# Performance work log

Measured on AMD Instinct MI355X. Metric: run time of the kernel, lower is better.

Reference implementation:

```python
import jax, jax.numpy as jnp
import numpy as np

A = 2048          # number of atoms
IN_DEPTH = 64
OUT_DEPTH = 64
FILTER_LEN = 12


def setup_inputs() -> dict:
    key = jax.random.key(0)
    k1, k2, k3, k4, k5 = jax.random.split(key, 5)
    node_property_tensor = jax.random.normal(k1, (A, IN_DEPTH), dtype=jnp.float32)
    # connectivity acts as a dense (soft) gather matrix: (A, A, FILTER_LEN)
    connectivity_tensor = jax.random.uniform(k2, (A, A, FILTER_LEN), dtype=jnp.float32)
    bond_property_tensor = jax.random.normal(k3, (A, FILTER_LEN, 2), dtype=jnp.float32)
    # parameters initialized as in the torch module: normal * 0.01
    property_filters = jax.random.normal(k4, (OUT_DEPTH, FILTER_LEN, IN_DEPTH), dtype=jnp.float32) * 0.01
    bond_filters = jax.random.normal(k5, (OUT_DEPTH, FILTER_LEN, 3), dtype=jnp.float32) * 0.01
    return {
        "node_property_tensor": node_property_tensor,
        "connectivity_tensor": connectivity_tensor,
        "bond_property_tensor": bond_property_tensor,
        "property_filters": property_filters,
        "bond_filters": bond_filters,
    }


def reference(node_property_tensor, connectivity_tensor, bond_property_tensor,
              property_filters, bond_filters):
    # node_connection[a, f, i] = sum_n conn[a, n, f] * x[n, i]
    node_connection = jnp.einsum('anf,ni->afi', connectivity_tensor, node_property_tensor)
    # bond_score[a, o, f] = sum_i node_connection[a, f, i] * property_filters[o, f, i]
    bond_score = jnp.einsum('afi,ofi->aof', node_connection, property_filters)
    # combined[a, o, f, :] = [bond_score, bond_prop0, bond_prop1]; multiply by
    # bond_filters[o, f, :] and sum over (f, channel). Split channel 0 (score)
    # from channels 1:3 (bond properties) to avoid materializing the concat.
    out = jnp.einsum('aof,of->ao', bond_score, bond_filters[:, :, 0])
    out = out + jnp.einsum('afc,ofc->ao', bond_property_tensor, bond_filters[:, :, 1:])
    return out  # (A, OUT_DEPTH)
```

## Files before the change

kernel.cpp:

```cpp
#include <hip/hip_runtime.h>


#define NATOM 2048
#define IN_D 64
#define OUT_D 64
#define FLEN 12
#define KTOT (NATOM * FLEN)
#define KSPLIT 32
#define KCHUNK (KTOT / KSPLIT)
#define BM 64
#define KS 64
#define NITER (KCHUNK / KS)
#define LDSW 72

typedef __attribute__((ext_vector_type(8))) short short8;
typedef __attribute__((ext_vector_type(4))) float f32x4;
typedef __attribute__((ext_vector_type(8))) unsigned short u16x8;
typedef __attribute__((ext_vector_type(4))) unsigned short u16x4;

__device__ __forceinline__ void split_bf16(float x, unsigned short& h, unsigned short& l) {
    unsigned int u = __builtin_bit_cast(unsigned int, x);
    unsigned int r = u + 0x7fffu + ((u >> 16) & 1u);
    h = (unsigned short)(r >> 16);
    float hf = __builtin_bit_cast(float, r & 0xffff0000u);
    float res = x - hf;
    unsigned int u2 = __builtin_bit_cast(unsigned int, res);
    l = (unsigned short)((u2 + 0x7fffu + ((u2 >> 16) & 1u)) >> 16);
}

__global__ __launch_bounds__(256) void compute_w_kernel(
    const float* __restrict__ x,
    const float* __restrict__ pf,
    const float* __restrict__ bf,
    unsigned short* __restrict__ wt_hi,
    unsigned short* __restrict__ wt_lo)
{
    __shared__ float x_lds[64][66];
    const int t = threadIdx.x;
    const int ob = blockIdx.x & 15;
    const int nb = blockIdx.x >> 4;

    {
        const int r = t >> 2;
        const int i0 = (t & 3) * 16;
        const float* src = x + (nb * 64 + r) * IN_D + i0;
        #pragma unroll
        for (int j = 0; j < 4; ++j) {
            float4 v = *(const float4*)(src + 4 * j);
            x_lds[r][i0 + 4 * j + 0] = v.x;
            x_lds[r][i0 + 4 * j + 1] = v.y;
            x_lds[r][i0 + 4 * j + 2] = v.z;
            x_lds[r][i0 + 4 * j + 3] = v.w;
        }
    }
    __syncthreads();

    const int l = t & 63;
    const int o = ob * 4 + (t >> 6);
    const int n = nb * 64 + l;

    float acc[FLEN];
    #pragma unroll
    for (int f = 0; f < FLEN; ++f) acc[f] = 0.f;

    for (int i = 0; i < IN_D; i += 4) {
        float x0 = x_lds[l][i + 0], x1 = x_lds[l][i + 1];
        float x2 = x_lds[l][i + 2], x3 = x_lds[l][i + 3];
        #pragma unroll
        for (int f = 0; f < FLEN; ++f) {
            float4 p = *(const float4*)(pf + (o * FLEN + f) * IN_D + i);
            acc[f] += p.x * x0 + p.y * x1 + p.z * x2 + p.w * x3;
        }
    }

    unsigned short hi[FLEN], lo[FLEN];
    #pragma unroll
    for (int f = 0; f < FLEN; ++f) {
        float wv = acc[f] * bf[(o * FLEN + f) * 3 + 0];
        split_bf16(wv, hi[f], lo[f]);
    }
    unsigned short* dh = wt_hi + o * KTOT + n * FLEN;
    unsigned short* dl = wt_lo + o * KTOT + n * FLEN;
    #pragma unroll
    for (int q = 0; q < 3; ++q) {
        u16x4 vh = { hi[4*q], hi[4*q+1], hi[4*q+2], hi[4*q+3] };
        u16x4 vl = { lo[4*q], lo[4*q+1], lo[4*q+2], lo[4*q+3] };
        *(u16x4*)(dh + 4 * q) = vh;
        *(u16x4*)(dl + 4 * q) = vl;
    }
}

__global__ __launch_bounds__(256, 4) void main_gemm_kernel(
    const float* __restrict__ conn,
    const unsigned short* __restrict__ wt_hi,
    const unsigned short* __restrict__ wt_lo,
    float* __restrict__ partials)
{
    __shared__ unsigned short lds[4][BM][LDSW];

    const int t = threadIdx.x;
    const int mblk = blockIdx.x & 31;
    const int kblk = blockIdx.x >> 5;
    const int mBase = mblk * BM;
    const int kBase = kblk * KCHUNK;

    const int r = t >> 2;
    const int p = t & 3;
    const int l = t & 63;
    const int w = t >> 6;
    const int lr = l & 15;
    const int g = l >> 4;

    f32x4 acc[4];
    #pragma unroll
    for (int nbt = 0; nbt < 4; ++nbt) acc[nbt] = 0.f;

    const float* connRow = conn + (long)(mBase + r) * KTOT + kBase;
    const unsigned short* whRow = wt_hi + r * KTOT + kBase;
    const unsigned short* wlRow = wt_lo + r * KTOT + kBase;

    #pragma unroll 1
    for (int it = 0; it < NITER; ++it) {
        const int kOff = it * KS;
        #pragma unroll
        for (int j = 0; j < 4; ++j) {
            const int kq = p * 4 + j * 16;
            float4 v = *(const float4*)(connRow + kOff + kq);
            unsigned short h0, h1, h2, h3, l0, l1, l2, l3;
            split_bf16(v.x, h0, l0);
            split_bf16(v.y, h1, l1);
            split_bf16(v.z, h2, l2);
            split_bf16(v.w, h3, l3);
            u16x4 h = { h0, h1, h2, h3 };
            u16x4 lo = { l0, l1, l2, l3 };
            *(u16x4*)&lds[0][r][kq] = h;
            *(u16x4*)&lds[1][r][kq] = lo;
        }
        #pragma unroll
        for (int j2 = 0; j2 < 2; ++j2) {
            const int ko = p * 16 + j2 * 8;
            *(u16x8*)&lds[2][r][ko] = *(const u16x8*)(whRow + kOff + ko);
            *(u16x8*)&lds[3][r][ko] = *(const u16x8*)(wlRow + kOff + ko);
        }
        __syncthreads();
        #pragma unroll
        for (int kk = 0; kk < 2; ++kk) {
            const int ke = kk * 32 + g * 8;
            short8 ah = *(const short8*)&lds[0][16 * w + lr][ke];
            short8 al = *(const short8*)&lds[1][16 * w + lr][ke];
            #pragma unroll
            for (int nbt = 0; nbt < 4; ++nbt) {
                short8 bh = *(const short8*)&lds[2][16 * nbt + lr][ke];
                short8 bl = *(const short8*)&lds[3][16 * nbt + lr][ke];
                acc[nbt] = __builtin_amdgcn_mfma_f32_16x16x32_bf16(al, bh, acc[nbt], 0, 0, 0);
                acc[nbt] = __builtin_amdgcn_mfma_f32_16x16x32_bf16(ah, bl, acc[nbt], 0, 0, 0);
                acc[nbt] = __builtin_amdgcn_mfma_f32_16x16x32_bf16(ah, bh, acc[nbt], 0, 0, 0);
            }
        }
        __syncthreads();
    }

    float* dst = partials + (long)kblk * (NATOM * OUT_D);
    #pragma unroll
    for (int nbt = 0; nbt < 4; ++nbt) {
        #pragma unroll
        for (int rr = 0; rr < 4; ++rr) {
            const int a = mBase + 16 * w + g * 4 + rr;
            const int o = nbt * 16 + lr;
            dst[a * OUT_D + o] = acc[nbt][rr];
        }
    }
}

__global__ __launch_bounds__(256) void reduce_kernel(
    const float* __restrict__ partials,
    const float* __restrict__ bond,
    const float* __restrict__ bf,
    float* __restrict__ out)
{
    const int idx = blockIdx.x * 256 + threadIdx.x;
    const int a = idx >> 6;
    const int o = idx & 63;
    float s = 0.f;
    #pragma unroll
    for (int kb = 0; kb < KSPLIT; ++kb)
        s += partials[(long)kb * (NATOM * OUT_D) + idx];
    const float* brow = bond + a * (FLEN * 2);
    #pragma unroll
    for (int f = 0; f < FLEN; ++f) {
        s += brow[2 * f + 0] * bf[(o * FLEN + f) * 3 + 1];
        s += brow[2 * f + 1] * bf[(o * FLEN + f) * 3 + 2];
    }
    out[idx] = s;
}

extern "C" void kernel_launch(void* const* d_in, const int* in_sizes, int n_in,
                              void* d_out, int out_size, void* d_ws, size_t ws_size,
                              hipStream_t stream) {
    const float* x    = (const float*)d_in[0];
    const float* conn = (const float*)d_in[1];
    const float* bond = (const float*)d_in[2];
    const float* pf   = (const float*)d_in[3];
    const float* bf   = (const float*)d_in[4];
    float* out = (float*)d_out;

    unsigned short* wt_hi = (unsigned short*)d_ws;
    unsigned short* wt_lo = wt_hi + (size_t)OUT_D * KTOT;
    float* partials = (float*)(wt_lo + (size_t)OUT_D * KTOT);

    compute_w_kernel<<<512, 256, 0, stream>>>(x, pf, bf, wt_hi, wt_lo);
    main_gemm_kernel<<<1024, 256, 0, stream>>>(conn, wt_hi, wt_lo, partials);
    reduce_kernel<<<512, 256, 0, stream>>>(partials, bond, bf, out);
}
```

Before: 315.0 us.

## Load GEMM tiles directly to LDS with XOR swizzle and split bf16 after read

The main GEMM now uses global_load_lds to stream fp32 connectivity and the bf16 weight tiles straight into LDS, using XOR-swizzled layouts instead of register staging. The hi/lo bf16 split of the connectivity values moves to after the LDS read. Workgroup IDs are remapped across XCDs, and the reduce kernel is vectorized to float4. This is meant to cut register round-trips and VGPR pressure on the load path and improve cache locality. In exchange, each wave repeats the split work per read, and there is still no double buffering.

```diff
diff --git a/kernel.cpp b/kernel.cpp
--- a/kernel.cpp
+++ b/kernel.cpp
@@ -11,21 +11,25 @@
 #define BM 64
 #define KS 64
 #define NITER (KCHUNK / KS)
-#define LDSW 72
 
 typedef __attribute__((ext_vector_type(8))) short short8;
 typedef __attribute__((ext_vector_type(4))) float f32x4;
-typedef __attribute__((ext_vector_type(8))) unsigned short u16x8;
 typedef __attribute__((ext_vector_type(4))) unsigned short u16x4;
 
-__device__ __forceinline__ void split_bf16(float x, unsigned short& h, unsigned short& l) {
-    unsigned int u = __builtin_bit_cast(unsigned int, x);
-    unsigned int r = u + 0x7fffu + ((u >> 16) & 1u);
-    h = (unsigned short)(r >> 16);
+__device__ __forceinline__ void split2(float x, short& h, short& l) {
+    unsigned u = __builtin_bit_cast(unsigned, x);
+    unsigned r = u + 0x7fffu + ((u >> 16) & 1u);
+    h = (short)(r >> 16);
     float hf = __builtin_bit_cast(float, r & 0xffff0000u);
     float res = x - hf;
-    unsigned int u2 = __builtin_bit_cast(unsigned int, res);
-    l = (unsigned short)((u2 + 0x7fffu + ((u2 >> 16) & 1u)) >> 16);
+    unsigned u2 = __builtin_bit_cast(unsigned, res);
+    l = (short)((u2 + 0x7fffu + ((u2 >> 16) & 1u)) >> 16);
+}
+
+__device__ __forceinline__ void gll16(const void* g, void* l) {
+    __builtin_amdgcn_global_load_lds(
+        (__attribute__((address_space(1))) void*)g,
+        (__attribute__((address_space(3))) void*)l, 16, 0, 0);
 }
 
 __global__ __launch_bounds__(256) void compute_w_kernel(
@@ -73,18 +77,20 @@
         }
     }
 
-    unsigned short hi[FLEN], lo[FLEN];
+    short hi[FLEN], lo[FLEN];
     #pragma unroll
     for (int f = 0; f < FLEN; ++f) {
         float wv = acc[f] * bf[(o * FLEN + f) * 3 + 0];
-        split_bf16(wv, hi[f], lo[f]);
+        split2(wv, hi[f], lo[f]);
     }
     unsigned short* dh = wt_hi + o * KTOT + n * FLEN;
     unsigned short* dl = wt_lo + o * KTOT + n * FLEN;
     #pragma unroll
     for (int q = 0; q < 3; ++q) {
-        u16x4 vh = { hi[4*q], hi[4*q+1], hi[4*q+2], hi[4*q+3] };
-        u16x4 vl = { lo[4*q], lo[4*q+1], lo[4*q+2], lo[4*q+3] };
+        u16x4 vh = { (unsigned short)hi[4*q], (unsigned short)hi[4*q+1],
+                     (unsigned short)hi[4*q+2], (unsigned short)hi[4*q+3] };
+        u16x4 vl = { (unsigned short)lo[4*q], (unsigned short)lo[4*q+1],
+                     (unsigned short)lo[4*q+2], (unsigned short)lo[4*q+3] };
         *(u16x4*)(dh + 4 * q) = vh;
         *(u16x4*)(dl + 4 * q) = vl;
     }
@@ -96,62 +102,81 @@
     const unsigned short* __restrict__ wt_lo,
     float* __restrict__ partials)
 {
-    __shared__ unsigned short lds[4][BM][LDSW];
+    __shared__ float ldsA[BM * KS];
+    __shared__ unsigned short ldsBh[OUT_D * KS];
+    __shared__ unsigned short ldsBl[OUT_D * KS];
 
     const int t = threadIdx.x;
-    const int mblk = blockIdx.x & 31;
-    const int kblk = blockIdx.x >> 5;
+    const int bid = blockIdx.x;
+    const int wg = (bid & 7) * 128 + (bid >> 3);
+    const int mblk = wg & 31;
+    const int kblk = wg >> 5;
     const int mBase = mblk * BM;
     const int kBase = kblk * KCHUNK;
 
-    const int r = t >> 2;
-    const int p = t & 3;
-    const int l = t & 63;
+    const int lane = t & 63;
     const int w = t >> 6;
-    const int lr = l & 15;
-    const int g = l >> 4;
+    const int lr = lane & 15;
+    const int g = lane >> 4;
+
+    const float* pA[4];
+    #pragma unroll
+    for (int c = 0; c < 4; ++c) {
+        int s = w * 256 + c * 64 + lane;
+        int R = s >> 4, cc = s & 15;
+        int sc = cc ^ (R & 15);
+        pA[c] = conn + (size_t)(mBase + R) * KTOT + kBase + sc * 4;
+    }
+    const unsigned short* pBh[2];
+    const unsigned short* pBl[2];
+    #pragma unroll
+    for (int c = 0; c < 2; ++c) {
+        int s = w * 128 + c * 64 + lane;
+        int o = s >> 3, cc = s & 7;
+        int sc = cc ^ (o & 7);
+        pBh[c] = wt_hi + o * KTOT + kBase + sc * 8;
+        pBl[c] = wt_lo + o * KTOT + kBase + sc * 8;
+    }
 
     f32x4 acc[4];
     #pragma unroll
     for (int nbt = 0; nbt < 4; ++nbt) acc[nbt] = 0.f;
 
-    const float* connRow = conn + (long)(mBase + r) * KTOT + kBase;
-    const unsigned short* whRow = wt_hi + r * KTOT + kBase;
-    const unsigned short* wlRow = wt_lo + r * KTOT + kBase;
-
+    const int rowA = (16 * w + lr) * KS;
     #pragma unroll 1
     for (int it = 0; it < NITER; ++it) {
-        const int kOff = it * KS;
-        #pragma unroll
-        for (int j = 0; j < 4; ++j) {
-            const int kq = p * 4 + j * 16;
-            float4 v = *(const float4*)(connRow + kOff + kq);
-            unsigned short h0, h1, h2, h3, l0, l1, l2, l3;
-            split_bf16(v.x, h0, l0);
-            split_bf16(v.y, h1, l1);
-            split_bf16(v.z, h2, l2);
-            split_bf16(v.w, h3, l3);
-            u16x4 h = { h0, h1, h2, h3 };
-            u16x4 lo = { l0, l1, l2, l3 };
-            *(u16x4*)&lds[0][r][kq] = h;
-            *(u16x4*)&lds[1][r][kq] = lo;
-        }
-        #pragma unroll
-        for (int j2 = 0; j2 < 2; ++j2) {
-            const int ko = p * 16 + j2 * 8;
-            *(u16x8*)&lds[2][r][ko] = *(const u16x8*)(whRow + kOff + ko);
-            *(u16x8*)&lds[3][r][ko] = *(const u16x8*)(wlRow + kOff + ko);
+        const int kO = it * KS;
+        #pragma unroll
+        for (int c = 0; c < 4; ++c)
+            gll16(pA[c] + kO, &ldsA[w * 1024 + c * 256]);
+        #pragma unroll
+        for (int c = 0; c < 2; ++c) {
+            gll16(pBh[c] + kO, &ldsBh[(w * 128 + c * 64) * 8]);
+            gll16(pBl[c] + kO, &ldsBl[(w * 128 + c * 64) * 8]);
         }
         __syncthreads();
+
         #pragma unroll
         for (int kk = 0; kk < 2; ++kk) {
-            const int ke = kk * 32 + g * 8;
-            short8 ah = *(const short8*)&lds[0][16 * w + lr][ke];
-            short8 al = *(const short8*)&lds[1][16 * w + lr][ke];
+            const int cg0 = kk * 8 + g * 2;
+            float4 fa0 = *(const float4*)&ldsA[rowA + ((cg0    ) ^ lr) * 4];
+            float4 fa1 = *(const float4*)&ldsA[rowA + ((cg0 + 1) ^ lr) * 4];
+            short8 ah, al;
+            short hh, ll;
+            split2(fa0.x, hh, ll); ah[0] = hh; al[0] = ll;
+            split2(fa0.y, hh, ll); ah[1] = hh; al[1] = ll;
+            split2(fa0.z, hh, ll); ah[2] = hh; al[2] = ll;
+            split2(fa0.w, hh, ll); ah[3] = hh; al[3] = ll;
+            split2(fa1.x, hh, ll); ah[4] = hh; al[4] = ll;
+            split2(fa1.y, hh, ll); ah[5] = hh; al[5] = ll;
+            split2(fa1.z, hh, ll); ah[6] = hh; al[6] = ll;
+            split2(fa1.w, hh, ll); ah[7] = hh; al[7] = ll;
             #pragma unroll
             for (int nbt = 0; nbt < 4; ++nbt) {
-                short8 bh = *(const short8*)&lds[2][16 * nbt + lr][ke];
-                short8 bl = *(const short8*)&lds[3][16 * nbt + lr][ke];
+                const int o = 16 * nbt + lr;
+                const int bidx = (o * 8 + ((kk * 4 + g) ^ (lr & 7))) * 8;
+                short8 bh = *(const short8*)&ldsBh[bidx];
+                short8 bl = *(const short8*)&ldsBl[bidx];
                 acc[nbt] = __builtin_amdgcn_mfma_f32_16x16x32_bf16(al, bh, acc[nbt], 0, 0, 0);
                 acc[nbt] = __builtin_amdgcn_mfma_f32_16x16x32_bf16(ah, bl, acc[nbt], 0, 0, 0);
                 acc[nbt] = __builtin_amdgcn_mfma_f32_16x16x32_bf16(ah, bh, acc[nbt], 0, 0, 0);
@@ -160,7 +185,7 @@
         __syncthreads();
     }
 
-    float* dst = partials + (long)kblk * (NATOM * OUT_D);
+    float* dst = partials + (size_t)kblk * (NATOM * OUT_D);
     #pragma unroll
     for (int nbt = 0; nbt < 4; ++nbt) {
         #pragma unroll
@@ -178,20 +203,28 @@
     const float* __restrict__ bf,
     float* __restrict__ out)
 {
-    const int idx = blockIdx.x * 256 + threadIdx.x;
-    const int a = idx >> 6;
-    const int o = idx & 63;
-    float s = 0.f;
-    #pragma unroll
-    for (int kb = 0; kb < KSPLIT; ++kb)
-        s += partials[(long)kb * (NATOM * OUT_D) + idx];
+    const int t4 = blockIdx.x * 256 + threadIdx.x;
+    const int e0 = t4 * 4;
+    const int a = e0 >> 6;
+    const int o0 = e0 & 63;
+
+    float4 s = *(const float4*)&partials[e0];
+    #pragma unroll
+    for (int kb = 1; kb < KSPLIT; ++kb) {
+        float4 p = *(const float4*)&partials[(size_t)kb * (NATOM * OUT_D) + e0];
+        s.x += p.x; s.y += p.y; s.z += p.z; s.w += p.w;
+    }
     const float* brow = bond + a * (FLEN * 2);
     #pragma unroll
     for (int f = 0; f < FLEN; ++f) {
-        s += brow[2 * f + 0] * bf[(o * FLEN + f) * 3 + 1];
-        s += brow[2 * f + 1] * bf[(o * FLEN + f) * 3 + 2];
-    }
-    out[idx] = s;
+        const float b0 = brow[2 * f + 0];
+        const float b1 = brow[2 * f + 1];
+        s.x += b0 * bf[((o0 + 0) * FLEN + f) * 3 + 1] + b1 * bf[((o0 + 0) * FLEN + f) * 3 + 2];
+        s.y += b0 * bf[((o0 + 1) * FLEN + f) * 3 + 1] + b1 * bf[((o0 + 1) * FLEN + f) * 3 + 2];
+        s.z += b0 * bf[((o0 + 2) * FLEN + f) * 3 + 1] + b1 * bf[((o0 + 2) * FLEN + f) * 3 + 2];
+        s.w += b0 * bf[((o0 + 3) * FLEN + f) * 3 + 1] + b1 * bf[((o0 + 3) * FLEN + f) * 3 + 2];
+    }
+    *(float4*)&out[e0] = s;
 }
 
 extern "C" void kernel_launch(void* const* d_in, const int* in_sizes, int n_in,
@@ -210,5 +243,5 @@
 
     compute_w_kernel<<<512, 256, 0, stream>>>(x, pf, bf, wt_hi, wt_lo);
     main_gemm_kernel<<<1024, 256, 0, stream>>>(conn, wt_hi, wt_lo, partials);
-    reduce_kernel<<<512, 256, 0, stream>>>(partials, bond, bf, out);
-}
+    reduce_kernel<<<128, 256, 0, stream>>>(partials, bond, bf, out);
+}
```

New measurement: 318.2 us. Within noise of the previous version (+1.0%).
